# Performance work log

Hardware: AMD Instinct MI355X
Metric: run time of the kernel (lower is better)

Reference implementation:

```python
import jax, jax.numpy as jnp
import numpy as np

# Perfect-tree regularization of the recursive UpDownVec graph:
#   T tactics per internal node, S siblings per tactic, L levels, branching B = T*S.
T, S, L = 2, 4, 7
B = T * S
DIM = 128
EPS = 1.0  # epsilon in AggChildrenVec
SIZES = [B ** l for l in range(L)]          # nodes per level: 1, 8, ..., 262144
OFFS = np.concatenate([[0], np.cumsum(SIZES)])
N_TOTAL = int(OFFS[-1])                      # 299593


def setup_inputs() -> dict:
    key = jax.random.key(0)
    ks = jax.random.split(key, 12)
    sc = 1.0 / np.sqrt(DIM)
    return {
        "initial_vecs": jax.random.normal(ks[0], (N_TOTAL, DIM), jnp.float32),
        "Ws": jax.random.normal(ks[1], (DIM, DIM), jnp.float32) * sc,
        "bs": jax.random.normal(ks[2], (DIM,), jnp.float32) * sc,
        "Wc": jax.random.normal(ks[3], (DIM, DIM), jnp.float32) * sc,
        "bc": jax.random.normal(ks[4], (DIM,), jnp.float32) * sc,
        "Wx": jax.random.normal(ks[5], (DIM, DIM), jnp.float32) * sc,
        "bx": jax.random.normal(ks[6], (DIM,), jnp.float32) * sc,
        "Wf": jax.random.normal(ks[7], (DIM, 2 * DIM), jnp.float32) * sc,
        "bf": jax.random.normal(ks[8], (DIM,), jnp.float32) * sc,
        "Wh": jax.random.normal(ks[9], (1, DIM), jnp.float32) * sc,
        "bh": jax.random.normal(ks[10], (1,), jnp.float32) * sc,
    }


def reference(initial_vecs, Ws, bs, Wc, bc, Wx, bx, Wf, bf, Wh, bh):
    dim = initial_vecs.shape[-1]
    init = [initial_vecs[OFFS[l]:OFFS[l + 1]] for l in range(L)]  # static slices

    # ---- up_step (bottom-up): leaves -> root ----
    agg = [None] * L
    agg[L - 1] = init[L - 1]                                    # leaves: agg = initial
    for l in range(L - 2, -1, -1):
        ch = agg[l + 1].reshape(SIZES[l], T, S, dim)            # children agg vecs
        # AggSiblingsVec: mean over siblings of relu(linear)
        sib_h = jax.nn.relu(jnp.einsum('ntsd,ed->ntse', ch, Ws) + bs)
        sib_agg = sib_h.mean(axis=2)                            # [n, T, dim]
        # AggChildrenVec: node + eps * mean over tactics of relu(linear)
        ch_h = jax.nn.relu(jnp.einsum('ntd,ed->nte', sib_agg, Wc) + bc)
        agg[l] = init[l] + EPS * ch_h.mean(axis=1)

    # ---- down_step (top-down): root -> leaves ----
    ctx = [None] * L
    ctx[0] = jnp.ones((1, dim), initial_vecs.dtype)             # root context = ones
    for l in range(L - 1):
        # AggContextVec over cat([parent_ctx, other_siblings_agg]); mean is
        # order-invariant so set-based sibling gathering is reproduced exactly.
        h = jax.nn.relu(agg[l + 1] @ Wx.T + bx).reshape(SIZES[l], T, S, dim)
        sum_h = h.sum(axis=2)                                   # [n, T, dim]
        ctx_h = jax.nn.relu(ctx[l] @ Wx.T + bx)                 # [n, dim]
        child_ctx = (ctx_h[:, None, None, :] + sum_h[:, :, None, :] - h) / S
        ctx[l + 1] = child_ctx.reshape(SIZES[l + 1], dim)

    # ---- final_agg for every node ----
    ctx_all = jnp.concatenate(ctx, axis=0)                      # [N, dim]
    agg_all = jnp.concatenate(agg, axis=0)                      # [N, dim]
    x = jnp.concatenate([ctx_all, agg_all], axis=1)             # [N, 2*dim]
    x = jax.nn.relu(x @ Wf.T + bf)
    return x @ Wh.T + bh                                        # [N, 1]
```

## Files before the change

### kernel.cpp

```cpp
#include <hip/hip_runtime.h>
#include <stdint.h>

#define DIM 128
#define LPAD 136

static constexpr long long NTOT = 299593LL;

using bf16x8 = __attribute__((ext_vector_type(8))) __bf16;
using f32x4  = __attribute__((ext_vector_type(4))) float;

__device__ __forceinline__ float relu(float x){ return x > 0.f ? x : 0.f; }
__device__ __forceinline__ __bf16 tobf(float x){ return (__bf16)x; }

__device__ __forceinline__ void mfma_acc(f32x4& acc, bf16x8 a, bf16x8 b){
    acc = __builtin_amdgcn_mfma_f32_16x16x32_bf16(a, b, acc, 0, 0, 0);
}

__device__ __forceinline__ void load_w_lds(const __bf16* __restrict__ wsrc,
                                           __bf16* lds, int src_stride){
    int t = threadIdx.x;
    #pragma unroll
    for (int i = 0; i < 8; ++i){
        int idx = t + i*256;
        int row = idx >> 4, col8 = (idx & 15) << 3;
        *(uint4*)(&lds[row*LPAD + col8]) = *(const uint4*)(wsrc + row*src_stride + col8);
    }
}

__global__ __launch_bounds__(256) void prep_kernel(
    const float* __restrict__ Ws, const float* __restrict__ Wc,
    const float* __restrict__ Wx, const float* __restrict__ Wf,
    __bf16* __restrict__ wts, __bf16* __restrict__ ctx)
{
    int idx = blockIdx.x*256 + threadIdx.x;
    if      (idx < 16384) wts[idx] = tobf(Ws[idx]);
    else if (idx < 32768) wts[idx] = tobf(Wc[idx - 16384]);
    else if (idx < 49152) wts[idx] = tobf(Wx[idx - 32768]);
    else if (idx < 81920) wts[idx] = tobf(Wf[idx - 49152]);
    else if (idx < 82048) ctx[idx - 81920] = tobf(1.0f);
}

template<bool LEAF>
__global__ __launch_bounds__(256, 3) void up_kernel(
    const __bf16* __restrict__ wts,
    const float* __restrict__ init,
    const float* __restrict__ bs, const float* __restrict__ bc,
    __bf16* __restrict__ agg,
    long long child_base, long long parent_base, long long n_par)
{
    __shared__ __bf16 lds_w[128*LPAD];
    __shared__ __bf16 lds_sib[32*LPAD];

    const int t = threadIdx.x;
    const int w = t >> 6, lane = t & 63, quad = lane >> 4, l15 = lane & 15;

    load_w_lds(wts, lds_w, 128);
    __syncthreads();

    const long long n_child = n_par * 8;
    const long long rowbase = (long long)blockIdx.x*128 + w*32;

    f32x4 acc[2][8];
    #pragma unroll
    for (int tt = 0; tt < 2; ++tt)
        #pragma unroll
        for (int i = 0; i < 8; ++i) acc[tt][i] = f32x4{0.f,0.f,0.f,0.f};

    bf16x8 af[2][4];
    #pragma unroll
    for (int tt = 0; tt < 2; ++tt){
        long long r = rowbase + tt*16 + l15;
        if (r >= n_child) r = n_child - 1;
        const long long base = (child_base + r)*DIM;
        #pragma unroll
        for (int ks = 0; ks < 4; ++ks){
            if (LEAF){
                const float* p = init + base + ks*32 + quad*8;
                float4 v0 = *(const float4*)p;
                float4 v1 = *(const float4*)(p + 4);
                bf16x8 a;
                a[0]=tobf(v0.x); a[1]=tobf(v0.y); a[2]=tobf(v0.z); a[3]=tobf(v0.w);
                a[4]=tobf(v1.x); a[5]=tobf(v1.y); a[6]=tobf(v1.z); a[7]=tobf(v1.w);
                af[tt][ks] = a;
                *(uint4*)(agg + base + ks*32 + quad*8) = *(uint4*)&a;
            } else {
                af[tt][ks] = *(const bf16x8*)(agg + base + ks*32 + quad*8);
            }
        }
    }
    #pragma unroll
    for (int ks = 0; ks < 4; ++ks){
        #pragma unroll
        for (int nt = 0; nt < 8; ++nt){
            bf16x8 bfrag = *(const bf16x8*)&lds_w[(nt*16 + l15)*LPAD + ks*32 + quad*8];
            mfma_acc(acc[0][nt], af[0][ks], bfrag);
            mfma_acc(acc[1][nt], af[1][ks], bfrag);
        }
    }
    #pragma unroll
    for (int tt = 0; tt < 2; ++tt){
        const int g = w*8 + tt*4 + quad;
        #pragma unroll
        for (int nt = 0; nt < 8; ++nt){
            int col = nt*16 + l15;
            float b = bs[col];
            float s = relu(acc[tt][nt][0]+b) + relu(acc[tt][nt][1]+b)
                    + relu(acc[tt][nt][2]+b) + relu(acc[tt][nt][3]+b);
            lds_sib[g*LPAD + col] = tobf(s * 0.25f);
        }
    }
    __syncthreads();
    load_w_lds(wts + 16384, lds_w, 128);
    __syncthreads();

    if (w < 2){
        f32x4 a2c[8];
        #pragma unroll
        for (int i = 0; i < 8; ++i) a2c[i] = f32x4{0.f,0.f,0.f,0.f};
        bf16x8 a2[4];
        #pragma unroll
        for (int ks = 0; ks < 4; ++ks)
            a2[ks] = *(const bf16x8*)&lds_sib[(w*16 + l15)*LPAD + ks*32 + quad*8];
        #pragma unroll
        for (int ks = 0; ks < 4; ++ks){
            #pragma unroll
            for (int nt = 0; nt < 8; ++nt){
                bf16x8 bfrag = *(const bf16x8*)&lds_w[(nt*16 + l15)*LPAD + ks*32 + quad*8];
                mfma_acc(a2c[nt], a2[ks], bfrag);
            }
        }
        const long long p0 = (long long)blockIdx.x*16 + w*8 + quad*2;
        const long long p1 = p0 + 1;
        #pragma unroll
        for (int nt = 0; nt < 8; ++nt){
            int col = nt*16 + l15;
            float b = bc[col];
            float r0 = relu(a2c[nt][0]+b), r1 = relu(a2c[nt][1]+b);
            float r2 = relu(a2c[nt][2]+b), r3 = relu(a2c[nt][3]+b);
            if (p0 < n_par){
                long long gr = parent_base + p0;
                agg[gr*DIM + col] = tobf(init[gr*DIM + col] + 0.5f*(r0+r1));
            }
            if (p1 < n_par){
                long long gr = parent_base + p1;
                agg[gr*DIM + col] = tobf(init[gr*DIM + col] + 0.5f*(r2+r3));
            }
        }
    }
}

__global__ __launch_bounds__(256, 3) void down_kernel(
    const __bf16* __restrict__ wts,
    const float* __restrict__ bx,
    const __bf16* __restrict__ agg,
    __bf16* __restrict__ ctx,
    long long parent_base, long long child_base, long long n_par)
{
    __shared__ __bf16 lds_w[128*LPAD];
    __shared__ float lds_ctxh[16*132];

    const int t = threadIdx.x;
    const int w = t >> 6, lane = t & 63, quad = lane >> 4, l15 = lane & 15;

    load_w_lds(wts + 32768, lds_w, 128);
    __syncthreads();

    const long long n_child = n_par*8;

    if (w == 0){
        f32x4 acc[8];
        #pragma unroll
        for (int i = 0; i < 8; ++i) acc[i] = f32x4{0.f,0.f,0.f,0.f};
        bf16x8 a[4];
        long long p = (long long)blockIdx.x*16 + l15;
        if (p >= n_par) p = n_par - 1;
        #pragma unroll
        for (int ks = 0; ks < 4; ++ks)
            a[ks] = *(const bf16x8*)(ctx + (parent_base + p)*DIM + ks*32 + quad*8);
        #pragma unroll
        for (int ks = 0; ks < 4; ++ks){
            #pragma unroll
            for (int nt = 0; nt < 8; ++nt){
                bf16x8 bfrag = *(const bf16x8*)&lds_w[(nt*16 + l15)*LPAD + ks*32 + quad*8];
                mfma_acc(acc[nt], a[ks], bfrag);
            }
        }
        #pragma unroll
        for (int nt = 0; nt < 8; ++nt){
            int col = nt*16 + l15;
            float b = bx[col];
            #pragma unroll
            for (int rg = 0; rg < 4; ++rg)
                lds_ctxh[(quad*4 + rg)*132 + col] = relu(acc[nt][rg] + b);
        }
    }
    __syncthreads();

    f32x4 acc[2][8];
    #pragma unroll
    for (int tt = 0; tt < 2; ++tt)
        #pragma unroll
        for (int i = 0; i < 8; ++i) acc[tt][i] = f32x4{0.f,0.f,0.f,0.f};
    bf16x8 a[2][4];
    const long long rowbase = (long long)blockIdx.x*128 + w*32;
    #pragma unroll
    for (int tt = 0; tt < 2; ++tt){
        long long r = rowbase + tt*16 + l15;
        if (r >= n_child) r = n_child - 1;
        #pragma unroll
        for (int ks = 0; ks < 4; ++ks)
            a[tt][ks] = *(const bf16x8*)(agg + (child_base + r)*DIM + ks*32 + quad*8);
    }
    #pragma unroll
    for (int ks = 0; ks < 4; ++ks){
        #pragma unroll
        for (int nt = 0; nt < 8; ++nt){
            bf16x8 bfrag = *(const bf16x8*)&lds_w[(nt*16 + l15)*LPAD + ks*32 + quad*8];
            mfma_acc(acc[0][nt], a[0][ks], bfrag);
            mfma_acc(acc[1][nt], a[1][ks], bfrag);
        }
    }
    #pragma unroll
    for (int tt = 0; tt < 2; ++tt){
        const long long rb = rowbase + tt*16 + quad*4;
        const int p_loc = w*4 + tt*2 + (quad >> 1);
        #pragma unroll
        for (int nt = 0; nt < 8; ++nt){
            int col = nt*16 + l15;
            float b = bx[col];
            float h0 = relu(acc[tt][nt][0]+b), h1 = relu(acc[tt][nt][1]+b);
            float h2 = relu(acc[tt][nt][2]+b), h3 = relu(acc[tt][nt][3]+b);
            float s = h0 + h1 + h2 + h3;
            float ch = lds_ctxh[p_loc*132 + col];
            if (rb   < n_child) ctx[(child_base + rb  )*DIM + col] = tobf((ch + s - h0)*0.25f);
            if (rb+1 < n_child) ctx[(child_base + rb+1)*DIM + col] = tobf((ch + s - h1)*0.25f);
            if (rb+2 < n_child) ctx[(child_base + rb+2)*DIM + col] = tobf((ch + s - h2)*0.25f);
            if (rb+3 < n_child) ctx[(child_base + rb+3)*DIM + col] = tobf((ch + s - h3)*0.25f);
        }
    }
}

__global__ __launch_bounds__(256, 3) void final_kernel(
    const __bf16* __restrict__ wts,
    const __bf16* __restrict__ ctx,
    const __bf16* __restrict__ agg,
    const float* __restrict__ bf_,
    const float* __restrict__ Wh, const float* __restrict__ bh,
    float* __restrict__ out)
{
    __shared__ __bf16 lds_w[128*LPAD];
    const int t = threadIdx.x;
    const int w = t >> 6, lane = t & 63, quad = lane >> 4, l15 = lane & 15;

    f32x4 acc[2][8];
    #pragma unroll
    for (int tt = 0; tt < 2; ++tt)
        #pragma unroll
        for (int i = 0; i < 8; ++i) acc[tt][i] = f32x4{0.f,0.f,0.f,0.f};

    const long long rowbase = (long long)blockIdx.x*128 + w*32;

    #pragma unroll
    for (int half = 0; half < 2; ++half){
        load_w_lds(wts + 49152 + half*128, lds_w, 256);
        __syncthreads();
        const __bf16* src = half ? agg : ctx;
        bf16x8 a[2][4];
        #pragma unroll
        for (int tt = 0; tt < 2; ++tt){
            long long r = rowbase + tt*16 + l15;
            if (r >= NTOT) r = NTOT - 1;
            #pragma unroll
            for (int ks = 0; ks < 4; ++ks)
                a[tt][ks] = *(const bf16x8*)(src + r*DIM + ks*32 + quad*8);
        }
        #pragma unroll
        for (int ks = 0; ks < 4; ++ks){
            #pragma unroll
            for (int nt = 0; nt < 8; ++nt){
                bf16x8 bfrag = *(const bf16x8*)&lds_w[(nt*16 + l15)*LPAD + ks*32 + quad*8];
                mfma_acc(acc[0][nt], a[0][ks], bfrag);
                mfma_acc(acc[1][nt], a[1][ks], bfrag);
            }
        }
        __syncthreads();
    }

    #pragma unroll
    for (int tt = 0; tt < 2; ++tt){
        float p0 = 0.f, p1 = 0.f, p2 = 0.f, p3 = 0.f;
        #pragma unroll
        for (int nt = 0; nt < 8; ++nt){
            int col = nt*16 + l15;
            float b = bf_[col], wh = Wh[col];
            p0 += relu(acc[tt][nt][0]+b)*wh;
            p1 += relu(acc[tt][nt][1]+b)*wh;
            p2 += relu(acc[tt][nt][2]+b)*wh;
            p3 += relu(acc[tt][nt][3]+b)*wh;
        }
        #pragma unroll
        for (int m = 1; m < 16; m <<= 1){
            p0 += __shfl_xor(p0, m);
            p1 += __shfl_xor(p1, m);
            p2 += __shfl_xor(p2, m);
            p3 += __shfl_xor(p3, m);
        }
        if (l15 == 0){
            float bb = bh[0];
            long long r = rowbase + tt*16 + quad*4;
            if (r   < NTOT) out[r  ] = p0 + bb;
            if (r+1 < NTOT) out[r+1] = p1 + bb;
            if (r+2 < NTOT) out[r+2] = p2 + bb;
            if (r+3 < NTOT) out[r+3] = p3 + bb;
        }
    }
}

extern "C" void kernel_launch(void* const* d_in, const int* in_sizes, int n_in,
                              void* d_out, int out_size, void* d_ws, size_t ws_size,
                              hipStream_t stream)
{
    const float* init = (const float*)d_in[0];
    const float* Ws  = (const float*)d_in[1];
    const float* bs  = (const float*)d_in[2];
    const float* Wc  = (const float*)d_in[3];
    const float* bc  = (const float*)d_in[4];
    const float* Wx  = (const float*)d_in[5];
    const float* bx  = (const float*)d_in[6];
    const float* Wf  = (const float*)d_in[7];
    const float* bff = (const float*)d_in[8];
    const float* Wh  = (const float*)d_in[9];
    const float* bh  = (const float*)d_in[10];
    float* out = (float*)d_out;

    __bf16* agg = (__bf16*)d_ws;
    __bf16* ctx = agg + NTOT*DIM;
    __bf16* wts = ctx + NTOT*DIM;

    static const long long SZ[7] = {1,8,64,512,4096,32768,262144};
    static const long long OF[8] = {0,1,9,73,585,4681,37449,299593};

    prep_kernel<<<dim3(321), dim3(256), 0, stream>>>(Ws, Wc, Wx, Wf, wts, ctx);

    for (int l = 5; l >= 0; --l){
        int blocks = (int)((SZ[l]*8 + 127)/128);
        if (l == 5)
            up_kernel<true><<<dim3(blocks), dim3(256), 0, stream>>>(
                wts, init, bs, bc, agg, OF[6], OF[5], SZ[5]);
        else
            up_kernel<false><<<dim3(blocks), dim3(256), 0, stream>>>(
                wts, init, bs, bc, agg, OF[l+1], OF[l], SZ[l]);
    }
    for (int l = 0; l < 6; ++l){
        int blocks = (int)((SZ[l]*8 + 127)/128);
        down_kernel<<<dim3(blocks), dim3(256), 0, stream>>>(
            wts, bx, agg, ctx, OF[l], OF[l+1], SZ[l]);
    }
    final_kernel<<<dim3((int)((NTOT + 127)/128)), dim3(256), 0, stream>>>(
        wts, ctx, agg, bff, Wh, bh, out);
}
```

Before: 424.5 us.

## Fuse final MLP head into down kernel and prefetch weights into registers

The separate final pass over all nodes is folded into each down-level kernel. The freshly computed child context tile is staged in LDS and fed straight into the Wf/Wh head along with the already-loaded agg rows. The leaf level therefore never writes ctx to global memory, and the final kernel no longer re-reads ctx and agg. The root's output is computed by a small dedicated kernel. Weight tiles and parent init values are prefetched into registers early to overlap global loads with compute, at the cost of more registers and LDS and lower occupancy (launch bound drops to 2 blocks).

Measured after the change: 502.0 us. +18.3%, slower.

```diff
diff --git a/kernel.cpp b/kernel.cpp
--- a/kernel.cpp
+++ b/kernel.cpp
@@ -24,6 +24,25 @@
         int idx = t + i*256;
         int row = idx >> 4, col8 = (idx & 15) << 3;
         *(uint4*)(&lds[row*LPAD + col8]) = *(const uint4*)(wsrc + row*src_stride + col8);
+    }
+}
+__device__ __forceinline__ void load_w_regs(const __bf16* __restrict__ wsrc,
+                                            uint4* wr, int src_stride){
+    int t = threadIdx.x;
+    #pragma unroll
+    for (int i = 0; i < 8; ++i){
+        int idx = t + i*256;
+        int row = idx >> 4, col8 = (idx & 15) << 3;
+        wr[i] = *(const uint4*)(wsrc + row*src_stride + col8);
+    }
+}
+__device__ __forceinline__ void store_w_regs(const uint4* wr, __bf16* lds){
+    int t = threadIdx.x;
+    #pragma unroll
+    for (int i = 0; i < 8; ++i){
+        int idx = t + i*256;
+        int row = idx >> 4, col8 = (idx & 15) << 3;
+        *(uint4*)(&lds[row*LPAD + col8]) = wr[i];
     }
 }
 
@@ -54,19 +73,11 @@
     const int t = threadIdx.x;
     const int w = t >> 6, lane = t & 63, quad = lane >> 4, l15 = lane & 15;
 
-    load_w_lds(wts, lds_w, 128);
-    __syncthreads();
-
     const long long n_child = n_par * 8;
     const long long rowbase = (long long)blockIdx.x*128 + w*32;
 
-    f32x4 acc[2][8];
-    #pragma unroll
-    for (int tt = 0; tt < 2; ++tt)
-        #pragma unroll
-        for (int i = 0; i < 8; ++i) acc[tt][i] = f32x4{0.f,0.f,0.f,0.f};
-
     bf16x8 af[2][4];
+    float4 v[2][4][2];
     #pragma unroll
     for (int tt = 0; tt < 2; ++tt){
         long long r = rowbase + tt*16 + l15;
@@ -76,18 +87,55 @@
         for (int ks = 0; ks < 4; ++ks){
             if (LEAF){
                 const float* p = init + base + ks*32 + quad*8;
-                float4 v0 = *(const float4*)p;
-                float4 v1 = *(const float4*)(p + 4);
-                bf16x8 a;
-                a[0]=tobf(v0.x); a[1]=tobf(v0.y); a[2]=tobf(v0.z); a[3]=tobf(v0.w);
-                a[4]=tobf(v1.x); a[5]=tobf(v1.y); a[6]=tobf(v1.z); a[7]=tobf(v1.w);
-                af[tt][ks] = a;
-                *(uint4*)(agg + base + ks*32 + quad*8) = *(uint4*)&a;
+                v[tt][ks][0] = *(const float4*)p;
+                v[tt][ks][1] = *(const float4*)(p + 4);
             } else {
                 af[tt][ks] = *(const bf16x8*)(agg + base + ks*32 + quad*8);
             }
         }
     }
+    float pinit[2][8];
+    const long long p0 = (long long)blockIdx.x*16 + w*8 + quad*2;
+    if (w < 2){
+        long long q0 = p0     < n_par ? p0     : n_par - 1;
+        long long q1 = p0 + 1 < n_par ? p0 + 1 : n_par - 1;
+        #pragma unroll
+        for (int nt = 0; nt < 8; ++nt){
+            int col = nt*16 + l15;
+            pinit[0][nt] = init[(parent_base + q0)*DIM + col];
+            pinit[1][nt] = init[(parent_base + q1)*DIM + col];
+        }
+    }
+    uint4 wcr[8];
+    if (!LEAF) load_w_regs(wts + 16384, wcr, 128);
+
+    load_w_lds(wts, lds_w, 128);
+
+    if (LEAF){
+        #pragma unroll
+        for (int tt = 0; tt < 2; ++tt){
+            long long r = rowbase + tt*16 + l15;
+            if (r >= n_child) r = n_child - 1;
+            const long long base = (child_base + r)*DIM;
+            #pragma unroll
+            for (int ks = 0; ks < 4; ++ks){
+                bf16x8 a;
+                a[0]=tobf(v[tt][ks][0].x); a[1]=tobf(v[tt][ks][0].y);
+                a[2]=tobf(v[tt][ks][0].z); a[3]=tobf(v[tt][ks][0].w);
+                a[4]=tobf(v[tt][ks][1].x); a[5]=tobf(v[tt][ks][1].y);
+                a[6]=tobf(v[tt][ks][1].z); a[7]=tobf(v[tt][ks][1].w);
+                af[tt][ks] = a;
+                *(uint4*)(agg + base + ks*32 + quad*8) = *(uint4*)&a;
+            }
+        }
+    }
+    __syncthreads();
+
+    f32x4 acc[2][8];
+    #pragma unroll
+    for (int tt = 0; tt < 2; ++tt)
+        #pragma unroll
+        for (int i = 0; i < 8; ++i) acc[tt][i] = f32x4{0.f,0.f,0.f,0.f};
     #pragma unroll
     for (int ks = 0; ks < 4; ++ks){
         #pragma unroll
@@ -110,7 +158,8 @@
         }
     }
     __syncthreads();
-    load_w_lds(wts + 16384, lds_w, 128);
+    if (LEAF) load_w_lds(wts + 16384, lds_w, 128);
+    else      store_w_regs(wcr, lds_w);
     __syncthreads();
 
     if (w < 2){
@@ -129,60 +178,73 @@
                 mfma_acc(a2c[nt], a2[ks], bfrag);
             }
         }
-        const long long p0 = (long long)blockIdx.x*16 + w*8 + quad*2;
-        const long long p1 = p0 + 1;
         #pragma unroll
         for (int nt = 0; nt < 8; ++nt){
             int col = nt*16 + l15;
             float b = bc[col];
-            float r0 = relu(a2c[nt][0]+b), r1 = relu(a2c[nt][1]+b);
-            float r2 = relu(a2c[nt][2]+b), r3 = relu(a2c[nt][3]+b);
-            if (p0 < n_par){
-                long long gr = parent_base + p0;
-                agg[gr*DIM + col] = tobf(init[gr*DIM + col] + 0.5f*(r0+r1));
-            }
-            if (p1 < n_par){
-                long long gr = parent_base + p1;
-                agg[gr*DIM + col] = tobf(init[gr*DIM + col] + 0.5f*(r2+r3));
-            }
-        }
-    }
-}
-
-__global__ __launch_bounds__(256, 3) void down_kernel(
+            float r01 = 0.5f*(relu(a2c[nt][0]+b) + relu(a2c[nt][1]+b));
+            float r23 = 0.5f*(relu(a2c[nt][2]+b) + relu(a2c[nt][3]+b));
+            if (p0 < n_par)
+                agg[(parent_base + p0)*DIM + col] = tobf(pinit[0][nt] + r01);
+            if (p0 + 1 < n_par)
+                agg[(parent_base + p0 + 1)*DIM + col] = tobf(pinit[1][nt] + r23);
+        }
+    }
+}
+
+template<bool WRITE_CTX>
+__global__ __launch_bounds__(256, 2) void down_kernel(
     const __bf16* __restrict__ wts,
     const float* __restrict__ bx,
     const __bf16* __restrict__ agg,
     __bf16* __restrict__ ctx,
+    const float* __restrict__ bf_,
+    const float* __restrict__ Wh, const float* __restrict__ bh,
+    float* __restrict__ out,
     long long parent_base, long long child_base, long long n_par)
 {
     __shared__ __bf16 lds_w[128*LPAD];
+    __shared__ __bf16 lds_tile[128*LPAD];
     __shared__ float lds_ctxh[16*132];
 
     const int t = threadIdx.x;
     const int w = t >> 6, lane = t & 63, quad = lane >> 4, l15 = lane & 15;
-
-    load_w_lds(wts + 32768, lds_w, 128);
-    __syncthreads();
-
     const long long n_child = n_par*8;
-
+    const long long rowbase = (long long)blockIdx.x*128 + w*32;
+
+    bf16x8 a[2][4];
+    #pragma unroll
+    for (int tt = 0; tt < 2; ++tt){
+        long long r = rowbase + tt*16 + l15;
+        if (r >= n_child) r = n_child - 1;
+        #pragma unroll
+        for (int ks = 0; ks < 4; ++ks)
+            a[tt][ks] = *(const bf16x8*)(agg + (child_base + r)*DIM + ks*32 + quad*8);
+    }
+    bf16x8 pc[4];
     if (w == 0){
-        f32x4 acc[8];
-        #pragma unroll
-        for (int i = 0; i < 8; ++i) acc[i] = f32x4{0.f,0.f,0.f,0.f};
-        bf16x8 a[4];
         long long p = (long long)blockIdx.x*16 + l15;
         if (p >= n_par) p = n_par - 1;
         #pragma unroll
         for (int ks = 0; ks < 4; ++ks)
-            a[ks] = *(const bf16x8*)(ctx + (parent_base + p)*DIM + ks*32 + quad*8);
+            pc[ks] = *(const bf16x8*)(ctx + (parent_base + p)*DIM + ks*32 + quad*8);
+    }
+    uint4 wfc[8], wfa[8];
+    load_w_regs(wts + 49152,       wfc, 256);
+    load_w_regs(wts + 49152 + 128, wfa, 256);
+    load_w_lds(wts + 32768, lds_w, 128);
+    __syncthreads();
+
+    if (w == 0){
+        f32x4 cacc[8];
+        #pragma unroll
+        for (int i = 0; i < 8; ++i) cacc[i] = f32x4{0.f,0.f,0.f,0.f};
         #pragma unroll
         for (int ks = 0; ks < 4; ++ks){
             #pragma unroll
             for (int nt = 0; nt < 8; ++nt){
                 bf16x8 bfrag = *(const bf16x8*)&lds_w[(nt*16 + l15)*LPAD + ks*32 + quad*8];
-                mfma_acc(acc[nt], a[ks], bfrag);
+                mfma_acc(cacc[nt], pc[ks], bfrag);
             }
         }
         #pragma unroll
@@ -191,26 +253,15 @@
             float b = bx[col];
             #pragma unroll
             for (int rg = 0; rg < 4; ++rg)
-                lds_ctxh[(quad*4 + rg)*132 + col] = relu(acc[nt][rg] + b);
-        }
-    }
-    __syncthreads();
+                lds_ctxh[(quad*4 + rg)*132 + col] = relu(cacc[nt][rg] + b);
+        }
+    }
 
     f32x4 acc[2][8];
     #pragma unroll
     for (int tt = 0; tt < 2; ++tt)
         #pragma unroll
         for (int i = 0; i < 8; ++i) acc[tt][i] = f32x4{0.f,0.f,0.f,0.f};
-    bf16x8 a[2][4];
-    const long long rowbase = (long long)blockIdx.x*128 + w*32;
-    #pragma unroll
-    for (int tt = 0; tt < 2; ++tt){
-        long long r = rowbase + tt*16 + l15;
-        if (r >= n_child) r = n_child - 1;
-        #pragma unroll
-        for (int ks = 0; ks < 4; ++ks)
-            a[tt][ks] = *(const bf16x8*)(agg + (child_base + r)*DIM + ks*32 + quad*8);
-    }
     #pragma unroll
     for (int ks = 0; ks < 4; ++ks){
         #pragma unroll
@@ -220,9 +271,12 @@
             mfma_acc(acc[1][nt], a[1][ks], bfrag);
         }
     }
+    __syncthreads();
+
     #pragma unroll
     for (int tt = 0; tt < 2; ++tt){
         const long long rb = rowbase + tt*16 + quad*4;
+        const int lrow = w*32 + tt*16 + quad*4;
         const int p_loc = w*4 + tt*2 + (quad >> 1);
         #pragma unroll
         for (int nt = 0; nt < 8; ++nt){
@@ -232,88 +286,102 @@
             float h2 = relu(acc[tt][nt][2]+b), h3 = relu(acc[tt][nt][3]+b);
             float s = h0 + h1 + h2 + h3;
             float ch = lds_ctxh[p_loc*132 + col];
-            if (rb   < n_child) ctx[(child_base + rb  )*DIM + col] = tobf((ch + s - h0)*0.25f);
-            if (rb+1 < n_child) ctx[(child_base + rb+1)*DIM + col] = tobf((ch + s - h1)*0.25f);
-            if (rb+2 < n_child) ctx[(child_base + rb+2)*DIM + col] = tobf((ch + s - h2)*0.25f);
-            if (rb+3 < n_child) ctx[(child_base + rb+3)*DIM + col] = tobf((ch + s - h3)*0.25f);
-        }
-    }
-}
-
-__global__ __launch_bounds__(256, 3) void final_kernel(
-    const __bf16* __restrict__ wts,
-    const __bf16* __restrict__ ctx,
-    const __bf16* __restrict__ agg,
-    const float* __restrict__ bf_,
-    const float* __restrict__ Wh, const float* __restrict__ bh,
-    float* __restrict__ out)
-{
-    __shared__ __bf16 lds_w[128*LPAD];
-    const int t = threadIdx.x;
-    const int w = t >> 6, lane = t & 63, quad = lane >> 4, l15 = lane & 15;
-
-    f32x4 acc[2][8];
+            float c0 = (ch + s - h0)*0.25f, c1 = (ch + s - h1)*0.25f;
+            float c2 = (ch + s - h2)*0.25f, c3 = (ch + s - h3)*0.25f;
+            lds_tile[(lrow+0)*LPAD + col] = tobf(c0);
+            lds_tile[(lrow+1)*LPAD + col] = tobf(c1);
+            lds_tile[(lrow+2)*LPAD + col] = tobf(c2);
+            lds_tile[(lrow+3)*LPAD + col] = tobf(c3);
+            if (WRITE_CTX){
+                if (rb   < n_child) ctx[(child_base + rb  )*DIM + col] = tobf(c0);
+                if (rb+1 < n_child) ctx[(child_base + rb+1)*DIM + col] = tobf(c1);
+                if (rb+2 < n_child) ctx[(child_base + rb+2)*DIM + col] = tobf(c2);
+                if (rb+3 < n_child) ctx[(child_base + rb+3)*DIM + col] = tobf(c3);
+            }
+        }
+    }
+    store_w_regs(wfc, lds_w);
+    __syncthreads();
+
     #pragma unroll
     for (int tt = 0; tt < 2; ++tt)
         #pragma unroll
         for (int i = 0; i < 8; ++i) acc[tt][i] = f32x4{0.f,0.f,0.f,0.f};
-
-    const long long rowbase = (long long)blockIdx.x*128 + w*32;
-
-    #pragma unroll
-    for (int half = 0; half < 2; ++half){
-        load_w_lds(wts + 49152 + half*128, lds_w, 256);
-        __syncthreads();
-        const __bf16* src = half ? agg : ctx;
-        bf16x8 a[2][4];
-        #pragma unroll
-        for (int tt = 0; tt < 2; ++tt){
-            long long r = rowbase + tt*16 + l15;
-            if (r >= NTOT) r = NTOT - 1;
-            #pragma unroll
-            for (int ks = 0; ks < 4; ++ks)
-                a[tt][ks] = *(const bf16x8*)(src + r*DIM + ks*32 + quad*8);
-        }
-        #pragma unroll
-        for (int ks = 0; ks < 4; ++ks){
-            #pragma unroll
-            for (int nt = 0; nt < 8; ++nt){
-                bf16x8 bfrag = *(const bf16x8*)&lds_w[(nt*16 + l15)*LPAD + ks*32 + quad*8];
-                mfma_acc(acc[0][nt], a[0][ks], bfrag);
-                mfma_acc(acc[1][nt], a[1][ks], bfrag);
-            }
-        }
-        __syncthreads();
-    }
-
+    bf16x8 ac[2][4];
+    #pragma unroll
+    for (int tt = 0; tt < 2; ++tt)
+        #pragma unroll
+        for (int ks = 0; ks < 4; ++ks)
+            ac[tt][ks] = *(const bf16x8*)&lds_tile[(w*32 + tt*16 + l15)*LPAD + ks*32 + quad*8];
+    #pragma unroll
+    for (int ks = 0; ks < 4; ++ks){
+        #pragma unroll
+        for (int nt = 0; nt < 8; ++nt){
+            bf16x8 bfrag = *(const bf16x8*)&lds_w[(nt*16 + l15)*LPAD + ks*32 + quad*8];
+            mfma_acc(acc[0][nt], ac[0][ks], bfrag);
+            mfma_acc(acc[1][nt], ac[1][ks], bfrag);
+        }
+    }
+    __syncthreads();
+    store_w_regs(wfa, lds_w);
+    __syncthreads();
+    #pragma unroll
+    for (int ks = 0; ks < 4; ++ks){
+        #pragma unroll
+        for (int nt = 0; nt < 8; ++nt){
+            bf16x8 bfrag = *(const bf16x8*)&lds_w[(nt*16 + l15)*LPAD + ks*32 + quad*8];
+            mfma_acc(acc[0][nt], a[0][ks], bfrag);
+            mfma_acc(acc[1][nt], a[1][ks], bfrag);
+        }
+    }
     #pragma unroll
     for (int tt = 0; tt < 2; ++tt){
-        float p0 = 0.f, p1 = 0.f, p2 = 0.f, p3 = 0.f;
+        float q0 = 0.f, q1 = 0.f, q2 = 0.f, q3 = 0.f;
         #pragma unroll
         for (int nt = 0; nt < 8; ++nt){
             int col = nt*16 + l15;
             float b = bf_[col], wh = Wh[col];
-            p0 += relu(acc[tt][nt][0]+b)*wh;
-            p1 += relu(acc[tt][nt][1]+b)*wh;
-            p2 += relu(acc[tt][nt][2]+b)*wh;
-            p3 += relu(acc[tt][nt][3]+b)*wh;
+            q0 += relu(acc[tt][nt][0]+b)*wh;
+            q1 += relu(acc[tt][nt][1]+b)*wh;
+            q2 += relu(acc[tt][nt][2]+b)*wh;
+            q3 += relu(acc[tt][nt][3]+b)*wh;
         }
         #pragma unroll
         for (int m = 1; m < 16; m <<= 1){
-            p0 += __shfl_xor(p0, m);
-            p1 += __shfl_xor(p1, m);
-            p2 += __shfl_xor(p2, m);
-            p3 += __shfl_xor(p3, m);
+            q0 += __shfl_xor(q0, m);
+            q1 += __shfl_xor(q1, m);
+            q2 += __shfl_xor(q2, m);
+            q3 += __shfl_xor(q3, m);
         }
         if (l15 == 0){
             float bb = bh[0];
             long long r = rowbase + tt*16 + quad*4;
-            if (r   < NTOT) out[r  ] = p0 + bb;
-            if (r+1 < NTOT) out[r+1] = p1 + bb;
-            if (r+2 < NTOT) out[r+2] = p2 + bb;
-            if (r+3 < NTOT) out[r+3] = p3 + bb;
-        }
-    }
+            if (r   < n_child) out[child_base + r  ] = q0 + bb;
+            if (r+1 < n_child) out[child_base + r+1] = q1 + bb;
+            if (r+2 < n_child) out[child_base + r+2] = q2 + bb;
+            if (r+3 < n_child) out[child_base + r+3] = q3 + bb;
+        }
+    }
+}
+
+__global__ __launch_bounds__(128) void root_final_kernel(
+    const float* __restrict__ Wf, const float* __restrict__ bf_,
+    const float* __restrict__ Wh, const float* __restrict__ bh,
+    const __bf16* __restrict__ agg, float* __restrict__ out)
+{
+    __shared__ float red[2];
+    int j = threadIdx.x;
+    float s = bf_[j];
+    #pragma unroll 4
+    for (int c = 0; c < 128; ++c) s += Wf[j*256 + c];
+    #pragma unroll 4
+    for (int c = 0; c < 128; ++c) s += Wf[j*256 + 128 + c] * (float)agg[c];
+    float x = relu(s) * Wh[j];
+    #pragma unroll
+    for (int m = 1; m < 64; m <<= 1) x += __shfl_xor(x, m);
+    if ((j & 63) == 0) red[j >> 6] = x;
+    __syncthreads();
+    if (j == 0) out[0] = red[0] + red[1] + bh[0];
 }
 
 extern "C" void kernel_launch(void* const* d_in, const int* in_sizes, int n_in,
@@ -351,11 +419,15 @@
             up_kernel<false><<<dim3(blocks), dim3(256), 0, stream>>>(
                 wts, init, bs, bc, agg, OF[l+1], OF[l], SZ[l]);
     }
+    root_final_kernel<<<dim3(1), dim3(128), 0, stream>>>(Wf, bff, Wh, bh, agg, out);
+
     for (int l = 0; l < 6; ++l){
         int blocks = (int)((SZ[l]*8 + 127)/128);
-        down_kernel<<<dim3(blocks), dim3(256), 0, stream>>>(
-            wts, bx, agg, ctx, OF[l], OF[l+1], SZ[l]);
-    }
-    final_kernel<<<dim3((int)((NTOT + 127)/128)), dim3(256), 0, stream>>>(
-        wts, ctx, agg, bff, Wh, bh, out);
-}
+        if (l == 5)
+            down_kernel<false><<<dim3(blocks), dim3(256), 0, stream>>>(
+                wts, bx, agg, ctx, bff, Wh, bh, out, OF[5], OF[6], SZ[5]);
+        else
+            down_kernel<true><<<dim3(blocks), dim3(256), 0, stream>>>(
+                wts, bx, agg, ctx, bff, Wh, bh, out, OF[l], OF[l+1], SZ[l]);
+    }
+}
```
